# Performance work log

Measured on AMD Instinct MI355X. Metric: run time of the kernel, lower is better.

## Reference

```python
import jax, jax.numpy as jnp
import numpy as np

N = 100000      # nodes
E = 1600000     # edges (avg degree 16)
DIN, DH, DOUT = 32, 48, 16


def _glorot(key, fan_in, fan_out):
    s = np.sqrt(6.0 / (fan_in + fan_out)).astype(np.float32)
    return jax.random.uniform(key, (fan_in, fan_out), jnp.float32, -s, s)


def setup_inputs() -> dict:
    key = jax.random.key(0)
    ks = jax.random.split(key, 6)
    x = jax.random.normal(ks[0], (N, DIN), jnp.float32)
    edge_index = jax.random.randint(ks[1], (2, E), 0, N, jnp.int32)
    return {
        "x": x,
        "edge_index": edge_index,
        "W1": _glorot(ks[2], DIN, DH), "b1": jnp.zeros((DH,), jnp.float32),
        "W2": _glorot(ks[3], DH, DH),  "b2": jnp.zeros((DH,), jnp.float32),
        "W3": _glorot(ks[4], DH, DOUT), "b3": jnp.zeros((DOUT,), jnp.float32),
    }


def reference(x, edge_index, W1, b1, W2, b2, W3, b3):
    # GCNConv with add_self_loops=True and symmetric normalization (gcn_norm).
    src, dst = edge_index[0], edge_index[1]
    loops = jnp.arange(N, dtype=src.dtype)
    src = jnp.concatenate([src, loops])  # [E+N]
    dst = jnp.concatenate([dst, loops])
    # in-degree at targets (edge weights are all ones)
    deg = jax.ops.segment_sum(jnp.ones(src.shape[0], jnp.float32), dst, num_segments=N)
    dinv = jnp.where(deg > 0, jax.lax.rsqrt(deg), 0.0)
    norm = dinv[src] * dinv[dst]  # [E+N]

    def conv(h, W, b):
        h = h @ W                          # [N, d_out] per-node linear
        m = h[src] * norm[:, None]         # gather + scale messages
        return jax.ops.segment_sum(m, dst, num_segments=N) + b  # scatter-add

    h = jax.nn.relu(conv(x, W1, b1))
    h = jax.nn.relu(conv(h, W2, b2))
    return conv(h, W3, b3)
```

## Files before the change

kernel.cpp:

```cpp
#include <hip/hip_runtime.h>


constexpr int Nn   = 100000;
constexpr int Ne   = 1600000;
constexpr int DIN  = 32;
constexpr int DH   = 48;
constexpr int DOUT = 16;
constexpr int TPB  = 256;

constexpr int BSH   = 7;
constexpr int NPBK  = 1 << BSH;
constexpr int NBUK  = (Nn + NPBK - 1) / NPBK;
constexpr int CAP   = 2560;
constexpr int EPB   = 4096;
constexpr int NBLKA = (Ne + EPB - 1) / EPB;

static inline int cdiv(long long a, long long b){ return (int)((a+b-1)/b); }
__device__ inline float4 ld4(const float* p){ return *reinterpret_cast<const float4*>(p); }


__global__ __launch_bounds__(1024) void initA_k(int* __restrict__ cursorA){
    int t = threadIdx.x;
    if (t < NBUK) cursorA[t] = t * CAP;
}

__global__ __launch_bounds__(TPB) void passA_k(const int* __restrict__ src,
                                               const int* __restrict__ dst,
                                               int* __restrict__ cursorA,
                                               int2* __restrict__ tmp){
    __shared__ int hist[NBUK];
    __shared__ int cbase[NBUK];
    const int t = threadIdx.x;
    for (int i = t; i < NBUK; i += TPB) hist[i] = 0;
    __syncthreads();
    const int e0 = blockIdx.x * EPB;
    const int e1 = min(e0 + EPB, Ne);
    for (int k = 0; k < EPB / (TPB * 4); ++k) {
        int e = e0 + k * (TPB * 4) + t * 4;
        if (e + 3 < e1) {
            int4 d4 = *reinterpret_cast<const int4*>(dst + e);
            atomicAdd(&hist[d4.x >> BSH], 1);
            atomicAdd(&hist[d4.y >> BSH], 1);
            atomicAdd(&hist[d4.z >> BSH], 1);
            atomicAdd(&hist[d4.w >> BSH], 1);
        } else {
            for (int j = 0; j < 4; ++j) { int ee = e + j; if (ee < e1) atomicAdd(&hist[dst[ee] >> BSH], 1); }
        }
    }
    __syncthreads();
    for (int b = t; b < NBUK; b += TPB) {
        int c = hist[b];
        cbase[b] = c ? atomicAdd(&cursorA[b], c) : 0;
        hist[b] = 0;
    }
    __syncthreads();
    for (int k = 0; k < EPB / (TPB * 4); ++k) {
        int e = e0 + k * (TPB * 4) + t * 4;
        if (e + 3 < e1) {
            int4 s4 = *reinterpret_cast<const int4*>(src + e);
            int4 d4 = *reinterpret_cast<const int4*>(dst + e);
            int b0 = d4.x >> BSH, b1 = d4.y >> BSH, b2 = d4.z >> BSH, b3 = d4.w >> BSH;
            int p0 = cbase[b0] + atomicAdd(&hist[b0], 1);
            int p1 = cbase[b1] + atomicAdd(&hist[b1], 1);
            int p2 = cbase[b2] + atomicAdd(&hist[b2], 1);
            int p3 = cbase[b3] + atomicAdd(&hist[b3], 1);
            if (p0 < (b0 + 1) * CAP) tmp[p0] = make_int2(s4.x, d4.x);
            if (p1 < (b1 + 1) * CAP) tmp[p1] = make_int2(s4.y, d4.y);
            if (p2 < (b2 + 1) * CAP) tmp[p2] = make_int2(s4.z, d4.z);
            if (p3 < (b3 + 1) * CAP) tmp[p3] = make_int2(s4.w, d4.w);
        } else {
            for (int j = 0; j < 4; ++j) {
                int ee = e + j;
                if (ee < e1) {
                    int s = src[ee], d = dst[ee];
                    int bb = d >> BSH;
                    int p = cbase[bb] + atomicAdd(&hist[bb], 1);
                    if (p < (bb + 1) * CAP) tmp[p] = make_int2(s, d);
                }
            }
        }
    }
}

__global__ __launch_bounds__(1024) void bucket_scan_k(const int* __restrict__ cursorA,
                                                      int* __restrict__ bucket_base,
                                                      int* __restrict__ rpN){
    __shared__ int s[1024];
    int t = threadIdx.x;
    int tot = (t < NBUK) ? (cursorA[t] - t * CAP) : 0;
    s[t] = tot;
    __syncthreads();
    for (int off = 1; off < 1024; off <<= 1) {
        int u = (t >= off) ? s[t - off] : 0;
        __syncthreads();
        s[t] += u;
        __syncthreads();
    }
    if (t < NBUK) bucket_base[t] = s[t] - tot;
    if (t == NBUK - 1) { bucket_base[NBUK] = s[t]; rpN[Nn] = s[t]; }
}

__global__ __launch_bounds__(TPB) void passB_k(const int2* __restrict__ tmp,
                                               const int* __restrict__ cursorA,
                                               const int* __restrict__ bucket_base,
                                               int* __restrict__ rpN,
                                               float* __restrict__ dinv,
                                               int* __restrict__ csr_src){
    __shared__ int ncnt[NPBK];
    __shared__ int s[NPBK];
    __shared__ int ncur[NPBK];
    const int t = threadIdx.x;
    const int b = blockIdx.x;
    const int e0 = b * CAP;
    const int e1 = min(cursorA[b], (b + 1) * CAP);
    const int cnt = e1 - e0;
    if (t < NPBK) ncnt[t] = 0;
    __syncthreads();
    for (int k = t; k < cnt; k += TPB) {
        int2 ed = tmp[e0 + k];
        atomicAdd(&ncnt[ed.y & (NPBK - 1)], 1);
    }
    __syncthreads();
    int my = 0;
    if (t < NPBK) { my = ncnt[t]; s[t] = my; }
    __syncthreads();
    for (int off = 1; off < NPBK; off <<= 1) {
        int u = 0;
        if (t < NPBK && t >= off) u = s[t - off];
        __syncthreads();
        if (t < NPBK) s[t] += u;
        __syncthreads();
    }
    if (t < NPBK) {
        int goff = bucket_base[b] + s[t] - my;
        ncur[t] = goff;
        int node = (b << BSH) + t;
        if (node < Nn) { rpN[node] = goff; dinv[node] = rsqrtf(1.0f + (float)my); }
    }
    __syncthreads();
    for (int k = t; k < cnt; k += TPB) {
        int2 ed = tmp[e0 + k];
        int pos = atomicAdd(&ncur[ed.y & (NPBK - 1)], 1);
        csr_src[pos] = ed.x;
    }
}

__global__ __launch_bounds__(TPB) void gather_x_k(const float* __restrict__ x,
                                                  const int* __restrict__ rpN,
                                                  const int* __restrict__ csr_src,
                                                  const float* __restrict__ dinv,
                                                  float* __restrict__ agg) {
    constexpr int G = DIN / 4;
    constexpr int NPB = TPB / G;
    const int local = threadIdx.x / G;
    const int f4    = threadIdx.x % G;
    const int i = blockIdx.x * NPB + local;
    if (i >= Nn) return;

    const int foff = f4 * 4;
    const float dni = dinv[i];
    float4 acc = ld4(x + (size_t)i * DIN + foff);
    acc.x *= dni; acc.y *= dni; acc.z *= dni; acc.w *= dni;

    const int beg = rpN[i];
    const int end = rpN[i + 1];
    int k = beg;
    for (; k + 3 < end; k += 4) {
        int s0 = csr_src[k];
        int s1 = csr_src[k + 1];
        int s2 = csr_src[k + 2];
        int s3 = csr_src[k + 3];
        float d0 = dinv[s0], d1 = dinv[s1], d2 = dinv[s2], d3 = dinv[s3];
        float4 v0 = ld4(x + (size_t)s0 * DIN + foff);
        float4 v1 = ld4(x + (size_t)s1 * DIN + foff);
        float4 v2 = ld4(x + (size_t)s2 * DIN + foff);
        float4 v3 = ld4(x + (size_t)s3 * DIN + foff);
        acc.x += v0.x * d0 + v1.x * d1 + v2.x * d2 + v3.x * d3;
        acc.y += v0.y * d0 + v1.y * d1 + v2.y * d2 + v3.y * d3;
        acc.z += v0.z * d0 + v1.z * d1 + v2.z * d2 + v3.z * d3;
        acc.w += v0.w * d0 + v1.w * d1 + v2.w * d2 + v3.w * d3;
    }
    for (; k < end; ++k) {
        int s0 = csr_src[k];
        float d0 = dinv[s0];
        float4 v0 = ld4(x + (size_t)s0 * DIN + foff);
        acc.x += v0.x * d0; acc.y += v0.y * d0; acc.z += v0.z * d0; acc.w += v0.w * d0;
    }

    float4 o;
    o.x = acc.x * dni; o.y = acc.y * dni; o.z = acc.z * dni; o.w = acc.w * dni;
    *reinterpret_cast<float4*>(agg + (size_t)i * DIN + foff) = o;
}

__global__ __launch_bounds__(TPB) void linear12_k(const float* __restrict__ agg,
                                                  const float* __restrict__ W1,
                                                  const float* __restrict__ b1,
                                                  const float* __restrict__ W2,
                                                  const float* __restrict__ dinv,
                                                  float* __restrict__ t2) {
    constexpr int PAD = DIN + 1;
    __shared__ float sW1[DIN * DH];
    __shared__ float sW2[DH * DH];
    __shared__ float sb1[DH];
    __shared__ float sh[TPB * PAD];
    const int t = threadIdx.x;
    const int base = blockIdx.x * TPB;

    for (int i = t; i < DIN * DH; i += TPB) sW1[i] = W1[i];
    for (int i = t; i < DH * DH; i += TPB) sW2[i] = W2[i];
    if (t < DH) sb1[t] = b1[t];
    for (int idx = t; idx < TPB * DIN; idx += TPB) {
        int g = base * DIN + idx;
        float v = (g < Nn * DIN) ? agg[g] : 0.0f;
        sh[(idx / DIN) * PAD + (idx % DIN)] = v;
    }
    __syncthreads();

    const int node = base + t;
    if (node >= Nn) return;

    float h1[DH];
#pragma unroll
    for (int j = 0; j < DH; ++j) h1[j] = sb1[j];
    for (int k = 0; k < DIN; ++k) {
        float a = sh[t * PAD + k];
#pragma unroll
        for (int j = 0; j < DH; ++j) h1[j] += a * sW1[k * DH + j];
    }
#pragma unroll
    for (int j = 0; j < DH; ++j) h1[j] = fmaxf(h1[j], 0.0f);

    float o[DH];
#pragma unroll
    for (int j = 0; j < DH; ++j) o[j] = 0.0f;
    for (int k = 0; k < DH; ++k) {
        float a = h1[k];
#pragma unroll
        for (int j = 0; j < DH; ++j) o[j] += a * sW2[k * DH + j];
    }
    const float dn = dinv[node];
    float* tp = t2 + (size_t)node * DH;
#pragma unroll
    for (int j = 0; j < DH; ++j) tp[j] = o[j] * dn;
}

template <int D_IN, int D_OUT, bool RELU>
__global__ __launch_bounds__(TPB) void linear_scale_k(const float* __restrict__ h,
                                                      const float* __restrict__ W,
                                                      const float* __restrict__ dinv,
                                                      float* __restrict__ t) {
    constexpr int PAD = D_IN + 1;
    __shared__ float sW[D_IN * D_OUT];
    __shared__ float sh[TPB * PAD];
    const int base = blockIdx.x * TPB;

    for (int idx = threadIdx.x; idx < D_IN * D_OUT; idx += TPB) sW[idx] = W[idx];
    for (int idx = threadIdx.x; idx < TPB * D_IN; idx += TPB) {
        int g = base * D_IN + idx;
        float v = (g < Nn * D_IN) ? h[g] : 0.0f;
        if (RELU) v = fmaxf(v, 0.0f);
        sh[(idx / D_IN) * PAD + (idx % D_IN)] = v;
    }
    __syncthreads();

    const int node = base + threadIdx.x;
    if (node >= Nn) return;

    float acc[D_OUT];
#pragma unroll
    for (int j = 0; j < D_OUT; ++j) acc[j] = 0.0f;
    for (int k = 0; k < D_IN; ++k) {
        float a = sh[threadIdx.x * PAD + k];
#pragma unroll
        for (int j = 0; j < D_OUT; ++j) acc[j] += a * sW[k * D_OUT + j];
    }
    float dn = dinv[node];
    float* tp = t + (size_t)node * D_OUT;
#pragma unroll
    for (int j = 0; j < D_OUT; ++j) tp[j] = acc[j] * dn;
}

template <int D, int G>
__global__ __launch_bounds__(TPB) void gather_k(const float* __restrict__ tp,
                                                const int* __restrict__ rpN,
                                                const int* __restrict__ csr_src,
                                                const float* __restrict__ dinv,
                                                const float* __restrict__ b,
                                                float* __restrict__ out) {
    constexpr int NPB = TPB / G;
    const int local = threadIdx.x / G;
    const int f4    = threadIdx.x % G;
    if (local >= NPB) return;
    const int i = blockIdx.x * NPB + local;
    if (i >= Nn) return;

    const int foff = f4 * 4;
    float4 acc = ld4(tp + (size_t)i * D + foff);
    const int beg = rpN[i];
    const int end = rpN[i + 1];

    int k = beg;
    for (; k + 3 < end; k += 4) {
        int s0 = csr_src[k];
        int s1 = csr_src[k + 1];
        int s2 = csr_src[k + 2];
        int s3 = csr_src[k + 3];
        float4 v0 = ld4(tp + (size_t)s0 * D + foff);
        float4 v1 = ld4(tp + (size_t)s1 * D + foff);
        float4 v2 = ld4(tp + (size_t)s2 * D + foff);
        float4 v3 = ld4(tp + (size_t)s3 * D + foff);
        acc.x += v0.x + v1.x + v2.x + v3.x;
        acc.y += v0.y + v1.y + v2.y + v3.y;
        acc.z += v0.z + v1.z + v2.z + v3.z;
        acc.w += v0.w + v1.w + v2.w + v3.w;
    }
    for (; k < end; ++k) {
        int s0 = csr_src[k];
        float4 v0 = ld4(tp + (size_t)s0 * D + foff);
        acc.x += v0.x; acc.y += v0.y; acc.z += v0.z; acc.w += v0.w;
    }

    const float dn = dinv[i];
    float4 bb = ld4(b + foff);
    float4 o;
    o.x = acc.x * dn + bb.x;
    o.y = acc.y * dn + bb.y;
    o.z = acc.z * dn + bb.z;
    o.w = acc.w * dn + bb.w;
    *reinterpret_cast<float4*>(out + (size_t)i * D + foff) = o;
}


extern "C" void kernel_launch(void* const* d_in, const int* in_sizes, int n_in,
                              void* d_out, int out_size, void* d_ws, size_t ws_size,
                              hipStream_t stream) {
    const float* x  = (const float*)d_in[0];
    const int*   ei = (const int*)d_in[1];
    const float* W1 = (const float*)d_in[2];
    const float* b1 = (const float*)d_in[3];
    const float* W2 = (const float*)d_in[4];
    const float* b2 = (const float*)d_in[5];
    const float* W3 = (const float*)d_in[6];
    const float* b3 = (const float*)d_in[7];
    const int* src = ei;
    const int* dst = ei + Ne;

    char* w = (char*)d_ws;
    int*   cursorA     = (int*)w;   w += 1024 * 4;
    int*   bucket_base = (int*)w;   w += 1024 * 4;
    int*   rpN         = (int*)w;   w += 100608L * 4;
    float* dinv        = (float*)w; w += 100352L * 4;
    int*   csr_src     = (int*)w;   w += 1600512L * 4;
    float* bufA        = (float*)w; w += (size_t)Nn * DH * 4;
    float* bufB        = (float*)w;
    int2*  tmp   = (int2*)bufA;
    float* t2    = bufA;
    float* t3    = bufA;
    float* agg32 = bufB;
    float* h2    = bufB;
    float* out   = (float*)d_out;

    initA_k<<<1, 1024, 0, stream>>>(cursorA);
    passA_k<<<NBLKA, TPB, 0, stream>>>(src, dst, cursorA, tmp);
    bucket_scan_k<<<1, 1024, 0, stream>>>(cursorA, bucket_base, rpN);
    passB_k<<<NBUK, TPB, 0, stream>>>(tmp, cursorA, bucket_base, rpN, dinv, csr_src);

    gather_x_k<<<cdiv(Nn, TPB / (DIN / 4)), TPB, 0, stream>>>(x, rpN, csr_src, dinv, agg32);
    linear12_k<<<cdiv(Nn, TPB), TPB, 0, stream>>>(agg32, W1, b1, W2, dinv, t2);

    gather_k<DH, 12><<<cdiv(Nn, TPB / 12), TPB, 0, stream>>>(t2, rpN, csr_src, dinv, b2, h2);

    linear_scale_k<DH, DOUT, true><<<cdiv(Nn, TPB), TPB, 0, stream>>>(h2, W3, dinv, t3);
    gather_k<DOUT, 4><<<cdiv(Nn, TPB / 4), TPB, 0, stream>>>(t3, rpN, csr_src, dinv, b3, out);
}
```

Before: 284.4 us.

## Store gathered node feature tables in fp16 to halve gather traffic

The node feature tables read by the three neighbour gathers (pre-scaled x, t2, t3) are now stored as fp16 and widened to fp32 on load, with fp32 accumulation. A new conv_x_k prescales x by dinv into fp16, so the first gather no longer loads per-neighbour dinv values. The aim is to halve the bytes moved by the random-access gathers, which dominate the runtime. In exchange it adds one extra pass over x and loses precision in the messages, which could push results past tolerance.

```diff
diff --git a/kernel.cpp b/kernel.cpp
--- a/kernel.cpp
+++ b/kernel.cpp
@@ -1,4 +1,5 @@
 #include <hip/hip_runtime.h>
+#include <hip/hip_fp16.h>
 
 
 constexpr int Nn   = 100000;
@@ -17,6 +18,16 @@
 
 static inline int cdiv(long long a, long long b){ return (int)((a+b-1)/b); }
 __device__ inline float4 ld4(const float* p){ return *reinterpret_cast<const float4*>(p); }
+
+__device__ inline void ld8h(const __half* p, float* v){
+    union { float4 f; __half2 h[4]; } u;
+    u.f = *reinterpret_cast<const float4*>(p);
+#pragma unroll
+    for (int q = 0; q < 4; ++q) {
+        float2 t = __half22float2(u.h[q]);
+        v[2*q] = t.x; v[2*q+1] = t.y;
+    }
+}
 
 
 __global__ __launch_bounds__(1024) void initA_k(int* __restrict__ cursorA){
@@ -145,51 +156,75 @@
     }
 }
 
-__global__ __launch_bounds__(TPB) void gather_x_k(const float* __restrict__ x,
+__global__ __launch_bounds__(TPB) void conv_x_k(const float* __restrict__ x,
+                                                const float* __restrict__ dinv,
+                                                __half* __restrict__ xh){
+    int g = blockIdx.x * TPB + threadIdx.x;
+    if (g >= Nn * (DIN / 8)) return;
+    int i  = g / (DIN / 8);
+    int j8 = (g % (DIN / 8)) * 8;
+    float dn = dinv[i];
+    float4 a = ld4(x + (size_t)i * DIN + j8);
+    float4 c = ld4(x + (size_t)i * DIN + j8 + 4);
+    union { float4 f; __half2 h[4]; } u;
+    u.h[0] = __floats2half2_rn(a.x * dn, a.y * dn);
+    u.h[1] = __floats2half2_rn(a.z * dn, a.w * dn);
+    u.h[2] = __floats2half2_rn(c.x * dn, c.y * dn);
+    u.h[3] = __floats2half2_rn(c.z * dn, c.w * dn);
+    *reinterpret_cast<float4*>(xh + (size_t)i * DIN + j8) = u.f;
+}
+
+template <int D, int G, bool BIAS>
+__global__ __launch_bounds__(TPB) void gather_h_k(const __half* __restrict__ tab,
                                                   const int* __restrict__ rpN,
                                                   const int* __restrict__ csr_src,
                                                   const float* __restrict__ dinv,
-                                                  float* __restrict__ agg) {
-    constexpr int G = DIN / 4;
+                                                  const float* __restrict__ b,
+                                                  float* __restrict__ out){
     constexpr int NPB = TPB / G;
     const int local = threadIdx.x / G;
-    const int f4    = threadIdx.x % G;
+    const int f8    = threadIdx.x % G;
+    if (local >= NPB) return;
     const int i = blockIdx.x * NPB + local;
     if (i >= Nn) return;
 
-    const int foff = f4 * 4;
-    const float dni = dinv[i];
-    float4 acc = ld4(x + (size_t)i * DIN + foff);
-    acc.x *= dni; acc.y *= dni; acc.z *= dni; acc.w *= dni;
+    const int hoff = f8 * 8;
+    float acc[8];
+    ld8h(tab + (size_t)i * D + hoff, acc);
 
     const int beg = rpN[i];
     const int end = rpN[i + 1];
     int k = beg;
-    for (; k + 3 < end; k += 4) {
+    float v0[8], v1[8];
+    for (; k + 1 < end; k += 2) {
         int s0 = csr_src[k];
         int s1 = csr_src[k + 1];
-        int s2 = csr_src[k + 2];
-        int s3 = csr_src[k + 3];
-        float d0 = dinv[s0], d1 = dinv[s1], d2 = dinv[s2], d3 = dinv[s3];
-        float4 v0 = ld4(x + (size_t)s0 * DIN + foff);
-        float4 v1 = ld4(x + (size_t)s1 * DIN + foff);
-        float4 v2 = ld4(x + (size_t)s2 * DIN + foff);
-        float4 v3 = ld4(x + (size_t)s3 * DIN + foff);
-        acc.x += v0.x * d0 + v1.x * d1 + v2.x * d2 + v3.x * d3;
-        acc.y += v0.y * d0 + v1.y * d1 + v2.y * d2 + v3.y * d3;
-        acc.z += v0.z * d0 + v1.z * d1 + v2.z * d2 + v3.z * d3;
-        acc.w += v0.w * d0 + v1.w * d1 + v2.w * d2 + v3.w * d3;
-    }
-    for (; k < end; ++k) {
+        ld8h(tab + (size_t)s0 * D + hoff, v0);
+        ld8h(tab + (size_t)s1 * D + hoff, v1);
+#pragma unroll
+        for (int q = 0; q < 8; ++q) acc[q] += v0[q] + v1[q];
+    }
+    if (k < end) {
         int s0 = csr_src[k];
-        float d0 = dinv[s0];
-        float4 v0 = ld4(x + (size_t)s0 * DIN + foff);
-        acc.x += v0.x * d0; acc.y += v0.y * d0; acc.z += v0.z * d0; acc.w += v0.w * d0;
-    }
-
-    float4 o;
-    o.x = acc.x * dni; o.y = acc.y * dni; o.z = acc.z * dni; o.w = acc.w * dni;
-    *reinterpret_cast<float4*>(agg + (size_t)i * DIN + foff) = o;
+        ld8h(tab + (size_t)s0 * D + hoff, v0);
+#pragma unroll
+        for (int q = 0; q < 8; ++q) acc[q] += v0[q];
+    }
+
+    const float dn = dinv[i];
+    float o[8];
+    if (BIAS) {
+        float4 ba = ld4(b + hoff);
+        float4 bc = ld4(b + hoff + 4);
+        o[0]=acc[0]*dn+ba.x; o[1]=acc[1]*dn+ba.y; o[2]=acc[2]*dn+ba.z; o[3]=acc[3]*dn+ba.w;
+        o[4]=acc[4]*dn+bc.x; o[5]=acc[5]*dn+bc.y; o[6]=acc[6]*dn+bc.z; o[7]=acc[7]*dn+bc.w;
+    } else {
+#pragma unroll
+        for (int q = 0; q < 8; ++q) o[q] = acc[q] * dn;
+    }
+    float* op = out + (size_t)i * D + hoff;
+    *reinterpret_cast<float4*>(op)     = make_float4(o[0], o[1], o[2], o[3]);
+    *reinterpret_cast<float4*>(op + 4) = make_float4(o[4], o[5], o[6], o[7]);
 }
 
 __global__ __launch_bounds__(TPB) void linear12_k(const float* __restrict__ agg,
@@ -197,7 +232,7 @@
                                                   const float* __restrict__ b1,
                                                   const float* __restrict__ W2,
                                                   const float* __restrict__ dinv,
-                                                  float* __restrict__ t2) {
+                                                  __half* __restrict__ t2h) {
     constexpr int PAD = DIN + 1;
     __shared__ float sW1[DIN * DH];
     __shared__ float sW2[DH * DH];
@@ -239,95 +274,45 @@
         for (int j = 0; j < DH; ++j) o[j] += a * sW2[k * DH + j];
     }
     const float dn = dinv[node];
-    float* tp = t2 + (size_t)node * DH;
-#pragma unroll
-    for (int j = 0; j < DH; ++j) tp[j] = o[j] * dn;
-}
-
-template <int D_IN, int D_OUT, bool RELU>
-__global__ __launch_bounds__(TPB) void linear_scale_k(const float* __restrict__ h,
-                                                      const float* __restrict__ W,
-                                                      const float* __restrict__ dinv,
-                                                      float* __restrict__ t) {
-    constexpr int PAD = D_IN + 1;
-    __shared__ float sW[D_IN * D_OUT];
+    __half2* tp = reinterpret_cast<__half2*>(t2h + (size_t)node * DH);
+#pragma unroll
+    for (int j = 0; j < DH / 2; ++j)
+        tp[j] = __floats2half2_rn(o[2*j] * dn, o[2*j+1] * dn);
+}
+
+__global__ __launch_bounds__(TPB) void linear3_k(const float* __restrict__ h,
+                                                 const float* __restrict__ W,
+                                                 const float* __restrict__ dinv,
+                                                 __half* __restrict__ t3h) {
+    constexpr int PAD = DH + 1;
+    __shared__ float sW[DH * DOUT];
     __shared__ float sh[TPB * PAD];
     const int base = blockIdx.x * TPB;
 
-    for (int idx = threadIdx.x; idx < D_IN * D_OUT; idx += TPB) sW[idx] = W[idx];
-    for (int idx = threadIdx.x; idx < TPB * D_IN; idx += TPB) {
-        int g = base * D_IN + idx;
-        float v = (g < Nn * D_IN) ? h[g] : 0.0f;
-        if (RELU) v = fmaxf(v, 0.0f);
-        sh[(idx / D_IN) * PAD + (idx % D_IN)] = v;
+    for (int idx = threadIdx.x; idx < DH * DOUT; idx += TPB) sW[idx] = W[idx];
+    for (int idx = threadIdx.x; idx < TPB * DH; idx += TPB) {
+        int g = base * DH + idx;
+        float v = (g < Nn * DH) ? h[g] : 0.0f;
+        sh[(idx / DH) * PAD + (idx % DH)] = fmaxf(v, 0.0f);
     }
     __syncthreads();
 
     const int node = base + threadIdx.x;
     if (node >= Nn) return;
 
-    float acc[D_OUT];
-#pragma unroll
-    for (int j = 0; j < D_OUT; ++j) acc[j] = 0.0f;
-    for (int k = 0; k < D_IN; ++k) {
+    float acc[DOUT];
+#pragma unroll
+    for (int j = 0; j < DOUT; ++j) acc[j] = 0.0f;
+    for (int k = 0; k < DH; ++k) {
         float a = sh[threadIdx.x * PAD + k];
 #pragma unroll
-        for (int j = 0; j < D_OUT; ++j) acc[j] += a * sW[k * D_OUT + j];
+        for (int j = 0; j < DOUT; ++j) acc[j] += a * sW[k * DOUT + j];
     }
     float dn = dinv[node];
-    float* tp = t + (size_t)node * D_OUT;
-#pragma unroll
-    for (int j = 0; j < D_OUT; ++j) tp[j] = acc[j] * dn;
-}
-
-template <int D, int G>
-__global__ __launch_bounds__(TPB) void gather_k(const float* __restrict__ tp,
-                                                const int* __restrict__ rpN,
-                                                const int* __restrict__ csr_src,
-                                                const float* __restrict__ dinv,
-                                                const float* __restrict__ b,
-                                                float* __restrict__ out) {
-    constexpr int NPB = TPB / G;
-    const int local = threadIdx.x / G;
-    const int f4    = threadIdx.x % G;
-    if (local >= NPB) return;
-    const int i = blockIdx.x * NPB + local;
-    if (i >= Nn) return;
-
-    const int foff = f4 * 4;
-    float4 acc = ld4(tp + (size_t)i * D + foff);
-    const int beg = rpN[i];
-    const int end = rpN[i + 1];
-
-    int k = beg;
-    for (; k + 3 < end; k += 4) {
-        int s0 = csr_src[k];
-        int s1 = csr_src[k + 1];
-        int s2 = csr_src[k + 2];
-        int s3 = csr_src[k + 3];
-        float4 v0 = ld4(tp + (size_t)s0 * D + foff);
-        float4 v1 = ld4(tp + (size_t)s1 * D + foff);
-        float4 v2 = ld4(tp + (size_t)s2 * D + foff);
-        float4 v3 = ld4(tp + (size_t)s3 * D + foff);
-        acc.x += v0.x + v1.x + v2.x + v3.x;
-        acc.y += v0.y + v1.y + v2.y + v3.y;
-        acc.z += v0.z + v1.z + v2.z + v3.z;
-        acc.w += v0.w + v1.w + v2.w + v3.w;
-    }
-    for (; k < end; ++k) {
-        int s0 = csr_src[k];
-        float4 v0 = ld4(tp + (size_t)s0 * D + foff);
-        acc.x += v0.x; acc.y += v0.y; acc.z += v0.z; acc.w += v0.w;
-    }
-
-    const float dn = dinv[i];
-    float4 bb = ld4(b + foff);
-    float4 o;
-    o.x = acc.x * dn + bb.x;
-    o.y = acc.y * dn + bb.y;
-    o.z = acc.z * dn + bb.z;
-    o.w = acc.w * dn + bb.w;
-    *reinterpret_cast<float4*>(out + (size_t)i * D + foff) = o;
+    __half2* tp = reinterpret_cast<__half2*>(t3h + (size_t)node * DOUT);
+#pragma unroll
+    for (int j = 0; j < DOUT / 2; ++j)
+        tp[j] = __floats2half2_rn(acc[2*j] * dn, acc[2*j+1] * dn);
 }
 
 
@@ -353,23 +338,25 @@
     int*   csr_src     = (int*)w;   w += 1600512L * 4;
     float* bufA        = (float*)w; w += (size_t)Nn * DH * 4;
     float* bufB        = (float*)w;
-    int2*  tmp   = (int2*)bufA;
-    float* t2    = bufA;
-    float* t3    = bufA;
-    float* agg32 = bufB;
-    float* h2    = bufB;
-    float* out   = (float*)d_out;
+    int2*   tmp   = (int2*)bufA;
+    __half* xh    = (__half*)bufA;
+    __half* t2h   = (__half*)bufA;
+    __half* t3h   = (__half*)bufA;
+    float*  agg32 = bufB;
+    float*  h2    = bufB;
+    float*  out   = (float*)d_out;
 
     initA_k<<<1, 1024, 0, stream>>>(cursorA);
     passA_k<<<NBLKA, TPB, 0, stream>>>(src, dst, cursorA, tmp);
     bucket_scan_k<<<1, 1024, 0, stream>>>(cursorA, bucket_base, rpN);
     passB_k<<<NBUK, TPB, 0, stream>>>(tmp, cursorA, bucket_base, rpN, dinv, csr_src);
 
-    gather_x_k<<<cdiv(Nn, TPB / (DIN / 4)), TPB, 0, stream>>>(x, rpN, csr_src, dinv, agg32);
-    linear12_k<<<cdiv(Nn, TPB), TPB, 0, stream>>>(agg32, W1, b1, W2, dinv, t2);
-
-    gather_k<DH, 12><<<cdiv(Nn, TPB / 12), TPB, 0, stream>>>(t2, rpN, csr_src, dinv, b2, h2);
-
-    linear_scale_k<DH, DOUT, true><<<cdiv(Nn, TPB), TPB, 0, stream>>>(h2, W3, dinv, t3);
-    gather_k<DOUT, 4><<<cdiv(Nn, TPB / 4), TPB, 0, stream>>>(t3, rpN, csr_src, dinv, b3, out);
-}
+    conv_x_k<<<cdiv((long long)Nn * (DIN / 8), TPB), TPB, 0, stream>>>(x, dinv, xh);
+    gather_h_k<DIN, DIN/8, false><<<cdiv(Nn, TPB/(DIN/8)), TPB, 0, stream>>>(xh, rpN, csr_src, dinv, nullptr, agg32);
+    linear12_k<<<cdiv(Nn, TPB), TPB, 0, stream>>>(agg32, W1, b1, W2, dinv, t2h);
+
+    gather_h_k<DH, DH/8, true><<<cdiv(Nn, TPB/(DH/8)), TPB, 0, stream>>>(t2h, rpN, csr_src, dinv, b2, h2);
+
+    linear3_k<<<cdiv(Nn, TPB), TPB, 0, stream>>>(h2, W3, dinv, t3h);
+    gather_h_k<DOUT, DOUT/8, true><<<cdiv(Nn, TPB/(DOUT/8)), TPB, 0, stream>>>(t3h, rpN, csr_src, dinv, b3, out);
+}
```

After: 265.1 us. -6.8%, faster.
